# Kernel optimization log

Hardware: AMD Instinct MI355X
Metric: run time of the kernel (lower is better)

The kernel has to match this reference:

```python
import jax, jax.numpy as jnp
import numpy as np

N_X, DIS, IN, OUT = 40000, 10000, 128, 64
N = N_X + DIS
E = 800000
BN_EPS = 1e-5


def setup_inputs() -> dict:
    key = jax.random.key(0)
    ks = jax.random.split(key, 20)

    def glorot(k, shape):
        fan_in, fan_out = shape[-2], shape[-1]
        a = np.sqrt(6.0 / (fan_in + fan_out)).astype(np.float32)
        return jax.random.uniform(k, shape, jnp.float32, -a, a)

    return {
        "x": jax.random.normal(ks[0], (N_X, IN), jnp.float32),
        "emb": jax.random.uniform(ks[1], (DIS, IN), jnp.float32),
        "conv1_w": glorot(ks[2], (3, IN, 2 * OUT)),
        "conv1_root": glorot(ks[3], (IN, 2 * OUT)),
        "conv1_bias": jnp.zeros((2 * OUT,), jnp.float32),
        "conv2_w": glorot(ks[4], (3, 2 * OUT, 4 * OUT)),
        "conv2_root": glorot(ks[5], (2 * OUT, 4 * OUT)),
        "conv2_bias": jnp.zeros((4 * OUT,), jnp.float32),
        "convinf_w": glorot(ks[6], (3, 4 * OUT, 4 * OUT)),
        "convinf_root": glorot(ks[7], (4 * OUT, 4 * OUT)),
        "convinf_bias": jnp.zeros((4 * OUT,), jnp.float32),
        "conv3_w": glorot(ks[8], (3, 4 * OUT, OUT)),
        "conv3_root": glorot(ks[9], (4 * OUT, OUT)),
        "conv3_bias": jnp.zeros((OUT,), jnp.float32),
        "norm1_g": jnp.ones((2 * OUT,), jnp.float32),
        "norm1_b": jnp.zeros((2 * OUT,), jnp.float32),
        "norm2_g": jnp.ones((4 * OUT,), jnp.float32),
        "norm2_b": jnp.zeros((4 * OUT,), jnp.float32),
        "edge_index": jax.random.randint(ks[10], (2, E), 0, N),
        "edge_types": jax.random.randint(ks[11], (E,), 0, 3),
    }


def reference(x, emb, conv1_w, conv1_root, conv1_bias, conv2_w, conv2_root,
              conv2_bias, convinf_w, convinf_root, convinf_bias, conv3_w,
              conv3_root, conv3_bias, norm1_g, norm1_b, norm2_g, norm2_b,
              edge_index, edge_types):
    dst, src = edge_index[0], edge_index[1]  # adj_t row = target, col = source
    n = x.shape[0] + emb.shape[0]

    # gcn_norm without self-loops: deg over rows, w_e = d^-1/2[dst] * d^-1/2[src]
    deg = jax.ops.segment_sum(jnp.ones(dst.shape[0], jnp.float32), dst, num_segments=n)
    dis = jnp.where(deg > 0, jax.lax.rsqrt(jnp.maximum(deg, 1.0)), 0.0)
    ew = dis[dst] * dis[src]  # [E]

    def wrgcn(h, W, root, bias):
        out = h @ root + bias
        h_src = h[src]  # [E, d] gather (dominant memory traffic)
        for r in range(3):
            w_r = jnp.where(edge_types == r, ew, 0.0)
            agg = jax.ops.segment_sum(w_r[:, None] * h_src, dst, num_segments=n)
            out = out + agg @ W[r]
        return out

    def bn(h, g, b):
        m = h.mean(axis=0)
        v = jnp.var(h, axis=0)  # biased, matches torch BN training normalization
        return (h - m) * jax.lax.rsqrt(v + BN_EPS) * g + b

    h0 = jnp.concatenate([x, emb], axis=0)  # [N, IN]
    x1 = bn(wrgcn(h0, conv1_w, conv1_root, conv1_bias), norm1_g, norm1_b)
    x2 = bn(wrgcn(jax.nn.relu(x1), conv2_w, conv2_root, conv2_bias), norm2_g, norm2_b)
    for _ in range(5):
        x2 = bn(wrgcn(jax.nn.relu(x2), convinf_w, convinf_root, convinf_bias), norm2_g, norm2_b)
    return wrgcn(jax.nn.relu(x2), conv3_w, conv3_root, conv3_bias)
```

## Files before the change

kernel.cpp:

```cpp
#include <hip/hip_runtime.h>

#define N_X  40000
#define NN   50000
#define NE   800000
#define MPAD 50048

using short8  = __attribute__((ext_vector_type(8))) short;
using floatx4 = __attribute__((ext_vector_type(4))) float;
using uintx2  = __attribute__((ext_vector_type(2))) unsigned int;
using uintx4  = __attribute__((ext_vector_type(4))) unsigned int;

typedef const __attribute__((address_space(1))) void gv_t;
typedef __attribute__((address_space(3))) void lv_t;

__device__ __forceinline__ unsigned short f2bf(float f) {
  unsigned u = __float_as_uint(f);
  u += 0x7FFF + ((u >> 16) & 1);
  return (unsigned short)(u >> 16);
}
__device__ __forceinline__ float bf2f(unsigned v) {
  return __uint_as_float(v << 16);
}
__device__ __forceinline__ float h2f(unsigned v) {
  unsigned short s = (unsigned short)v;
  _Float16 f;
  __builtin_memcpy(&f, &s, 2);
  return (float)f;
}
__device__ __forceinline__ unsigned short f2h(float f) {
  _Float16 h = (_Float16)f;
  unsigned short s;
  __builtin_memcpy(&s, &h, 2);
  return s;
}

__global__ void k_deg(const int* __restrict__ dst, int* __restrict__ deg) {
  int e = blockIdx.x * blockDim.x + threadIdx.x;
  if (e < NE) atomicAdd(&deg[dst[e]], 1);
}

__global__ void k_dis(const int* __restrict__ deg, float* __restrict__ dis) {
  int i = blockIdx.x * blockDim.x + threadIdx.x;
  if (i < NN) dis[i] = deg[i] > 0 ? rsqrtf((float)deg[i]) : 0.f;
}

#define SCAN_B 1024
#define SCAN_NB 49
__global__ void k_scan1(const int* __restrict__ deg, int* __restrict__ rowp,
                        int* __restrict__ bsum) {
  __shared__ int buf[SCAN_B];
  int b = blockIdx.x;
  int i = b * SCAN_B + threadIdx.x;
  int v = (i < NN) ? deg[i] : 0;
  buf[threadIdx.x] = v;
  __syncthreads();
  for (int off = 1; off < SCAN_B; off <<= 1) {
    int t = (threadIdx.x >= off) ? buf[threadIdx.x - off] : 0;
    __syncthreads();
    buf[threadIdx.x] += t;
    __syncthreads();
  }
  if (i < NN) rowp[i] = buf[threadIdx.x] - v;
  if (threadIdx.x == SCAN_B - 1) bsum[b] = buf[SCAN_B - 1];
}

__global__ void k_scan2(int* __restrict__ bsum) {
  if (threadIdx.x == 0) {
    int acc = 0;
    for (int i = 0; i < SCAN_NB; ++i) { int t = bsum[i]; bsum[i] = acc; acc += t; }
  }
}

__global__ void k_scan3(int* __restrict__ rowp, const int* __restrict__ bsum) {
  int i = blockIdx.x * blockDim.x + threadIdx.x;
  if (i < NN) rowp[i] += bsum[i >> 10];
  if (i == 0) rowp[NN] = NE;
}

__global__ void k_build(const int* __restrict__ dst, const int* __restrict__ src,
                        const int* __restrict__ typ, const float* __restrict__ dis,
                        const int* __restrict__ rowp, int* __restrict__ cur,
                        uintx2* __restrict__ ed) {
  int e = blockIdx.x * blockDim.x + threadIdx.x;
  if (e >= NE) return;
  int d = dst[e], s = src[e];
  int p = rowp[d] + atomicAdd(&cur[d], 1);
  uintx2 v;
  v.x = (unsigned)s | ((unsigned)typ[e] << 28);
  v.y = __float_as_uint(dis[d] * dis[s]);
  ed[p] = v;
}

__global__ void k_prep0(const float* __restrict__ x, const float* __restrict__ emb,
                        unsigned short* __restrict__ Gh, unsigned short* __restrict__ Gl) {
  int idx = blockIdx.x * blockDim.x + threadIdx.x;
  if (idx >= NN * 32) return;
  int r = idx >> 5;
  const float* srcp = (r < N_X) ? (x + (size_t)idx * 4)
                                : (emb + ((size_t)idx - (size_t)N_X * 32) * 4);
  float4 hv = *(const float4*)srcp;
  float vv[4] = {hv.x, hv.y, hv.z, hv.w};
  unsigned hw[2], lw[2];
#pragma unroll
  for (int q = 0; q < 2; ++q) {
    unsigned short h0 = f2bf(vv[2 * q]), h1 = f2bf(vv[2 * q + 1]);
    unsigned short l0 = f2bf(vv[2 * q] - bf2f(h0)), l1 = f2bf(vv[2 * q + 1] - bf2f(h1));
    hw[q] = (unsigned)h0 | ((unsigned)h1 << 16);
    lw[q] = (unsigned)l0 | ((unsigned)l1 << 16);
  }
  size_t o = (size_t)idx * 4;
  *(uintx2*)(Gh + o) = uintx2{hw[0], hw[1]};
  *(uintx2*)(Gl + o) = uintx2{lw[0], lw[1]};
}

__global__ void k_prep(const unsigned short* __restrict__ Hb,
                       const float* __restrict__ bns, const float* __restrict__ g,
                       const float* __restrict__ b, unsigned short* __restrict__ Gh,
                       unsigned short* __restrict__ Gl, int din) {
  int idx = blockIdx.x * blockDim.x + threadIdx.x;
  if (idx >= NN * (din >> 3)) return;
  int c8 = (idx & ((din >> 3) - 1)) * 8;
  uintx4 hv = *(const uintx4*)(Hb + (size_t)idx * 8);
  unsigned hwv[4] = {hv.x, hv.y, hv.z, hv.w};
  unsigned hw[4], lw[4];
#pragma unroll
  for (int q = 0; q < 4; ++q) {
    unsigned short oo[2];
#pragma unroll
    for (int p = 0; p < 2; ++p) {
      int c = c8 + 2 * q + p;
      float mean = bns[c] * (1.f / NN);
      float var = bns[din + c] * (1.f / NN) - mean * mean;
      float rs = rsqrtf(var + 1e-5f);
      float sc = rs * g[c];
      float sh = b[c] - mean * sc;
      float v = bf2f((hwv[q] >> (16 * p)) & 0xFFFFu);
      v = fmaxf(v * sc + sh, 0.f);
      oo[p] = f2bf(v);
      float lo = v - bf2f(oo[p]);
      if (p == 0) lw[q] = (unsigned)f2bf(lo);
      else        lw[q] |= ((unsigned)f2bf(lo) << 16);
    }
    hw[q] = (unsigned)oo[0] | ((unsigned)oo[1] << 16);
  }
  size_t o = (size_t)idx * 8;
  *(uintx4*)(Gh + o) = uintx4{hw[0], hw[1], hw[2], hw[3]};
  *(uintx4*)(Gl + o) = uintx4{lw[0], lw[1], lw[2], lw[3]};
}

__global__ void k_wcat2(const float* __restrict__ root, const float* __restrict__ W,
                        unsigned short* __restrict__ BhT, unsigned short* __restrict__ BlT,
                        int din, int dout) {
  int idx = blockIdx.x * blockDim.x + threadIdx.x;
  if (idx >= 4 * dout * din) return;
  int n = idx / din, k = idx % din;
  float v;
  if (n < dout) v = root[(size_t)k * dout + n];
  else {
    int r = n / dout - 1, c = n % dout;
    v = W[((size_t)r * din + k) * dout + c];
  }
  unsigned short h = f2bf(v);
  BhT[idx] = h;
  BlT[idx] = f2bf(v - bf2f(h));
}

__global__ __launch_bounds__(256, 2) void k_gemm2(
    const unsigned short* __restrict__ Ah, const unsigned short* __restrict__ Al,
    const unsigned short* __restrict__ Bh, const unsigned short* __restrict__ Bl,
    float* __restrict__ Rroot, unsigned short* __restrict__ P,
    int M, int K, int dout, int ny) {
  constexpr int TC = 40;
  constexpr int CPW = 10;
  constexpr int NT = 2;
  __shared__ __align__(16) char lds[2][TC * 1024];

  const int tid = threadIdx.x;
  const int lane = tid & 63;
  const int w = tid >> 6;
  const int wm = w >> 1, wn = w & 1;
  const int r16 = lane & 15, kg = lane >> 4;

  const int nwg = gridDim.x;
  const int q = nwg >> 3, r = nwg & 7;
  const int xcd = blockIdx.x & 7, pos = blockIdx.x >> 3;
  const int t = (xcd < r ? xcd * (q + 1) : r * (q + 1) + (xcd - r) * q) + pos;
  const int bm = (t / ny) * 256;
  const int bn = (t % ny) * 64;

  const int rowseg = lane >> 2;
  const int seg = (lane & 3) ^ ((lane >> 3) & 3);
  const unsigned short* gb[CPW];
#pragma unroll
  for (int i = 0; i < CPW; ++i) {
    int c = w * CPW + i;
    const unsigned short* base;
    int row0;
    if (c < 16)      { base = Ah; row0 = bm + c * 16; }
    else if (c < 32) { base = Al; row0 = bm + (c - 16) * 16; }
    else if (c < 36) { base = Bh; row0 = bn + (c - 32) * 16; }
    else             { base = Bl; row0 = bn + (c - 36) * 16; }
    gb[i] = base + (size_t)(row0 + rowseg) * K + seg * 8;
  }

  floatx4 acc[8][NT];
#pragma unroll
  for (int i = 0; i < 8; ++i)
#pragma unroll
    for (int jj = 0; jj < NT; ++jj) acc[i][jj] = (floatx4)0.f;

  const int nk = K >> 5;

  auto stage = [&](int b, int tk) {
#pragma unroll
    for (int i = 0; i < CPW; ++i)
      __builtin_amdgcn_global_load_lds((gv_t*)(gb[i] + tk * 32),
                                       (lv_t*)&lds[b][(w * CPW + i) * 1024],
                                       16, 0, 0);
  };

  stage(0, 0);
  stage(1, 1);

  const int fo = r16 * 64 + ((kg ^ ((r16 >> 1) & 3)) * 16);

  int buf = 0;
  for (int tk = 0; tk < nk; ++tk) {
    if (tk < nk - 1) asm volatile("s_waitcnt vmcnt(10)" ::: "memory");
    else             asm volatile("s_waitcnt vmcnt(0)" ::: "memory");
    __builtin_amdgcn_s_barrier();

    const char* Lb = lds[buf];
    short8 bh[NT], bl[NT];
#pragma unroll
    for (int nt = 0; nt < NT; ++nt) {
      bh[nt] = *(const short8*)(Lb + (32 + wn * NT + nt) * 1024 + fo);
      bl[nt] = *(const short8*)(Lb + (36 + wn * NT + nt) * 1024 + fo);
    }

    __builtin_amdgcn_s_setprio(1);
#pragma unroll
    for (int mt = 0; mt < 8; ++mt) {
      short8 ah = *(const short8*)(Lb + (wm * 8 + mt) * 1024 + fo);
      short8 al = *(const short8*)(Lb + (16 + wm * 8 + mt) * 1024 + fo);
#pragma unroll
      for (int nt = 0; nt < NT; ++nt) {
        acc[mt][nt] = __builtin_amdgcn_mfma_f32_16x16x32_bf16(ah, bh[nt], acc[mt][nt], 0, 0, 0);
        acc[mt][nt] = __builtin_amdgcn_mfma_f32_16x16x32_bf16(ah, bl[nt], acc[mt][nt], 0, 0, 0);
        acc[mt][nt] = __builtin_amdgcn_mfma_f32_16x16x32_bf16(al, bh[nt], acc[mt][nt], 0, 0, 0);
      }
    }
    __builtin_amdgcn_s_setprio(0);

    __builtin_amdgcn_s_barrier();
    if (tk + 2 < nk) stage(buf, tk + 2);
    buf ^= 1;
  }

  const int sec = bn / dout;
  const int cb = bn - sec * dout;
#pragma unroll
  for (int mt = 0; mt < 8; ++mt) {
    const int gr0 = bm + wm * 128 + mt * 16 + kg * 4;
#pragma unroll
    for (int nt = 0; nt < NT; ++nt) {
      const int colL = cb + wn * 32 + nt * 16 + r16;
#pragma unroll
      for (int rr = 0; rr < 4; ++rr) {
        const int gr = gr0 + rr;
        if (gr >= M) continue;
        const float o = acc[mt][nt][rr];
        if (sec == 0) Rroot[(size_t)gr * dout + colL] = o;
        else          P[((size_t)gr * 3 + (sec - 1)) * dout + colL] = f2h(o);
      }
    }
  }
}

template <int L, bool F32OUT>
__global__ void k_agg2(const unsigned short* __restrict__ P,
                       const float* __restrict__ Rroot,
                       const float* __restrict__ bias,
                       const int* __restrict__ rowp, const uintx2* __restrict__ ed,
                       void* __restrict__ OutV) {
  constexpr int G = 64 / L;
  constexpr int dout = L * 8;
  const int wid = (blockIdx.x * 256 + threadIdx.x) >> 6;
  if (wid >= NN) return;
  const int lane = threadIdx.x & 63;
  const int grp = lane / L;
  const int c0 = (lane & (L - 1)) * 8;
  const int beg = rowp[wid], end = rowp[wid + 1];
  float a[8] = {};
  for (int i = beg + grp; i < end; i += G) {
    const uintx2 e = ed[i];
    const float wv = __uint_as_float(e.y);
    const unsigned tt = e.x >> 28;
    const size_t off = ((size_t)(e.x & 0x0FFFFFFFu) * 3 + tt) * dout + c0;
    const uintx4 g = *(const uintx4*)(P + off);
    a[0] += wv * h2f(g.x & 0xFFFFu);
    a[1] += wv * h2f(g.x >> 16);
    a[2] += wv * h2f(g.y & 0xFFFFu);
    a[3] += wv * h2f(g.y >> 16);
    a[4] += wv * h2f(g.z & 0xFFFFu);
    a[5] += wv * h2f(g.z >> 16);
    a[6] += wv * h2f(g.w & 0xFFFFu);
    a[7] += wv * h2f(g.w >> 16);
  }
#pragma unroll
  for (int off = L; off < 64; off <<= 1) {
#pragma unroll
    for (int qq = 0; qq < 8; ++qq) a[qq] += __shfl_xor(a[qq], off);
  }
  if (grp == 0) {
    const size_t ob = (size_t)wid * dout + c0;
    const float4 bv0 = *(const float4*)(bias + c0);
    const float4 bv1 = *(const float4*)(bias + c0 + 4);
    const float4 rv0 = *(const float4*)(Rroot + ob);
    const float4 rv1 = *(const float4*)(Rroot + ob + 4);
    float o[8];
    o[0] = rv0.x + bv0.x + a[0];
    o[1] = rv0.y + bv0.y + a[1];
    o[2] = rv0.z + bv0.z + a[2];
    o[3] = rv0.w + bv0.w + a[3];
    o[4] = rv1.x + bv1.x + a[4];
    o[5] = rv1.y + bv1.y + a[5];
    o[6] = rv1.z + bv1.z + a[6];
    o[7] = rv1.w + bv1.w + a[7];
    if constexpr (F32OUT) {
      float* Out = (float*)OutV;
      *(float4*)(Out + ob) = make_float4(o[0], o[1], o[2], o[3]);
      *(float4*)(Out + ob + 4) = make_float4(o[4], o[5], o[6], o[7]);
    } else {
      unsigned short* Out = (unsigned short*)OutV;
      uintx4 pk;
      pk.x = (unsigned)f2bf(o[0]) | ((unsigned)f2bf(o[1]) << 16);
      pk.y = (unsigned)f2bf(o[2]) | ((unsigned)f2bf(o[3]) << 16);
      pk.z = (unsigned)f2bf(o[4]) | ((unsigned)f2bf(o[5]) << 16);
      pk.w = (unsigned)f2bf(o[6]) | ((unsigned)f2bf(o[7]) << 16);
      *(uintx4*)(Out + ob) = pk;
    }
  }
}

__global__ void k_bnstats(const unsigned short* __restrict__ Hb,
                          float* __restrict__ sums, int d) {
  __shared__ float ls[512];
  const int cg = d >> 3;
  const int rpb = 256 / cg;
  const int cgi = threadIdx.x & (cg - 1);
  const int rl = threadIdx.x / cg;
  const int c0 = cgi * 8;
  for (int i = threadIdx.x; i < 512; i += 256) ls[i] = 0.f;
  __syncthreads();

  float s[8] = {}, s2[8] = {};
  for (int row = blockIdx.x * rpb + rl; row < NN; row += gridDim.x * rpb) {
    uintx4 hv = *(const uintx4*)(Hb + (size_t)row * d + c0);
    unsigned wv[4] = {hv.x, hv.y, hv.z, hv.w};
#pragma unroll
    for (int q = 0; q < 4; ++q) {
      float v0 = bf2f(wv[q] & 0xFFFFu);
      float v1 = bf2f(wv[q] >> 16);
      s[2 * q] += v0;  s2[2 * q] += v0 * v0;
      s[2 * q + 1] += v1;  s2[2 * q + 1] += v1 * v1;
    }
  }
#pragma unroll
  for (int q = 0; q < 8; ++q) {
    atomicAdd(&ls[c0 + q], s[q]);
    atomicAdd(&ls[256 + c0 + q], s2[q]);
  }
  __syncthreads();
  if (threadIdx.x < d) {
    atomicAdd(&sums[threadIdx.x], ls[threadIdx.x]);
    atomicAdd(&sums[d + threadIdx.x], ls[256 + threadIdx.x]);
  }
}

extern "C" void kernel_launch(void* const* d_in, const int* in_sizes, int n_in,
                              void* d_out, int out_size, void* d_ws, size_t ws_size,
                              hipStream_t stream) {
  const float* x   = (const float*)d_in[0];
  const float* emb = (const float*)d_in[1];
  const float* conv_w[4] = {(const float*)d_in[2], (const float*)d_in[5],
                            (const float*)d_in[8], (const float*)d_in[11]};
  const float* conv_r[4] = {(const float*)d_in[3], (const float*)d_in[6],
                            (const float*)d_in[9], (const float*)d_in[12]};
  const float* conv_b[4] = {(const float*)d_in[4], (const float*)d_in[7],
                            (const float*)d_in[10], (const float*)d_in[13]};
  const float* n1g = (const float*)d_in[14];
  const float* n1b = (const float*)d_in[15];
  const float* n2g = (const float*)d_in[16];
  const float* n2b = (const float*)d_in[17];
  const int* eidx = (const int*)d_in[18];
  const int* etyp = (const int*)d_in[19];
  const int* dst  = eidx;
  const int* srcp = eidx + NE;
  float* out = (float*)d_out;

  char* w = (char*)d_ws;
  auto alloc = [&](size_t bytes) {
    char* p = w;
    w += (bytes + 255) & ~(size_t)255;
    return p;
  };
  unsigned short* Gh   = (unsigned short*)alloc((size_t)MPAD * 256 * 2);
  unsigned short* Gl   = (unsigned short*)alloc((size_t)MPAD * 256 * 2);
  unsigned short* P    = (unsigned short*)alloc((size_t)MPAD * 768 * 2);
  float*    Rroot = (float*)alloc((size_t)MPAD * 256 * 4);
  unsigned short* Hb = (unsigned short*)alloc((size_t)NN * 256 * 2);
  unsigned short* WTh[4];
  unsigned short* WTl[4];
  for (int i = 0; i < 4; ++i) {
    WTh[i] = (unsigned short*)alloc((size_t)1024 * 256 * 2);
    WTl[i] = (unsigned short*)alloc((size_t)1024 * 256 * 2);
  }
  float*    bns  = (float*)alloc(512 * 4);
  float*    dis  = (float*)alloc((size_t)NN * 4);
  int*      deg  = (int*)alloc((size_t)NN * 4);
  int*      rowp = (int*)alloc((size_t)(NN + 1) * 4);
  int*      cur  = (int*)alloc((size_t)NN * 4);
  int*      bsum = (int*)alloc(64 * 4);
  uintx2*   ed   = (uintx2*)alloc((size_t)NE * 8);

  hipMemsetAsync(deg, 0, (size_t)NN * 4, stream);
  hipMemsetAsync(cur, 0, (size_t)NN * 4, stream);
  k_deg<<<(NE + 255) / 256, 256, 0, stream>>>(dst, deg);
  k_dis<<<(NN + 255) / 256, 256, 0, stream>>>(deg, dis);
  k_scan1<<<SCAN_NB, SCAN_B, 0, stream>>>(deg, rowp, bsum);
  k_scan2<<<1, 64, 0, stream>>>(bsum);
  k_scan3<<<(NN + 255) / 256, 256, 0, stream>>>(rowp, bsum);
  k_build<<<(NE + 255) / 256, 256, 0, stream>>>(dst, srcp, etyp, dis, rowp, cur, ed);

  const int din_a[8]  = {128, 128, 256, 256, 256, 256, 256, 256};
  const int dout_a[8] = {128, 256, 256, 256, 256, 256, 256, 64};
  const int wi_a[8]   = {0, 1, 2, 2, 2, 2, 2, 3};
  const int gm = (MPAD + 255) / 256;

  const int wdin[4]  = {128, 128, 256, 256};
  const int wdout[4] = {128, 256, 256, 64};
  for (int i = 0; i < 4; ++i)
    k_wcat2<<<(4 * wdout[i] * wdin[i] + 255) / 256, 256, 0, stream>>>(
        conv_r[i], conv_w[i], WTh[i], WTl[i], wdin[i], wdout[i]);

  for (int l = 0; l < 8; ++l) {
    const int din = din_a[l], dout = dout_a[l];
    const int wi = wi_a[l];

    if (l == 0)
      k_prep0<<<(NN * 32 + 255) / 256, 256, 0, stream>>>(x, emb, Gh, Gl);
    else
      k_prep<<<(NN * (din >> 3) + 255) / 256, 256, 0, stream>>>(
          Hb, bns, (l == 1) ? n1g : n2g, (l == 1) ? n1b : n2b, Gh, Gl, din);

    const int ny = 4 * dout / 64;
    k_gemm2<<<gm * ny, 256, 0, stream>>>(Gh, Gl, WTh[wi], WTl[wi], Rroot, P, NN, din, dout, ny);

    if (l == 7) {
      k_agg2<8, true><<<(NN + 3) / 4, 256, 0, stream>>>(P, Rroot, conv_b[wi], rowp, ed, out);
    } else {
      if (dout == 256)
        k_agg2<32, false><<<(NN + 3) / 4, 256, 0, stream>>>(P, Rroot, conv_b[wi], rowp, ed, Hb);
      else
        k_agg2<16, false><<<(NN + 3) / 4, 256, 0, stream>>>(P, Rroot, conv_b[wi], rowp, ed, Hb);
      hipMemsetAsync(bns, 0, (size_t)2 * dout * 4, stream);
      k_bnstats<<<256, 256, 0, stream>>>(Hb, bns, dout);
    }
  }
}
```

Before: 1.488 ms.

## Widen GEMM tile to 256x128 with 512 threads and triple-buffered LDS

Replaces the 256x64 split-bf16 GEMM with a 256x128 tile run by 8 waves, a three-stage LDS ring buffer and a fully unrolled K loop templated on the K-tile count. Each K step is split into four phases that interleave fragment loads, prefetch of the next stage and MFMA bursts, with barriers between phases. The intent is to halve A-tile reloads per output column and overlap global loads with compute better. The cost is more LDS per block (one block per CU), extra barriers, and sector/column indexing computed per n-tile.

```diff
diff --git a/kernel.cpp b/kernel.cpp
--- a/kernel.cpp
+++ b/kernel.cpp
@@ -165,20 +165,21 @@
   BlT[idx] = f2bf(v - bf2f(h));
 }
 
-__global__ __launch_bounds__(256, 2) void k_gemm2(
+template <int NK>
+__global__ __launch_bounds__(512, 1) void k_gemm4(
     const unsigned short* __restrict__ Ah, const unsigned short* __restrict__ Al,
     const unsigned short* __restrict__ Bh, const unsigned short* __restrict__ Bl,
     float* __restrict__ Rroot, unsigned short* __restrict__ P,
-    int M, int K, int dout, int ny) {
-  constexpr int TC = 40;
-  constexpr int CPW = 10;
-  constexpr int NT = 2;
-  __shared__ __align__(16) char lds[2][TC * 1024];
+    int M, int dout, int ny) {
+  constexpr int K = NK * 32;
+  constexpr int TC = 48;
+  constexpr int CPW = 6;
+  __shared__ __align__(16) char lds[3][TC * 1024];
 
   const int tid = threadIdx.x;
   const int lane = tid & 63;
   const int w = tid >> 6;
-  const int wm = w >> 1, wn = w & 1;
+  const int wm = w >> 2, wn = w & 3;
   const int r16 = lane & 15, kg = lane >> 4;
 
   const int nwg = gridDim.x;
@@ -186,7 +187,7 @@
   const int xcd = blockIdx.x & 7, pos = blockIdx.x >> 3;
   const int t = (xcd < r ? xcd * (q + 1) : r * (q + 1) + (xcd - r) * q) + pos;
   const int bm = (t / ny) * 256;
-  const int bn = (t % ny) * 64;
+  const int bn = (t % ny) * 128;
 
   const int rowseg = lane >> 2;
   const int seg = (lane & 3) ^ ((lane >> 3) & 3);
@@ -198,18 +199,16 @@
     int row0;
     if (c < 16)      { base = Ah; row0 = bm + c * 16; }
     else if (c < 32) { base = Al; row0 = bm + (c - 16) * 16; }
-    else if (c < 36) { base = Bh; row0 = bn + (c - 32) * 16; }
-    else             { base = Bl; row0 = bn + (c - 36) * 16; }
+    else if (c < 40) { base = Bh; row0 = bn + (c - 32) * 16; }
+    else             { base = Bl; row0 = bn + (c - 40) * 16; }
     gb[i] = base + (size_t)(row0 + rowseg) * K + seg * 8;
   }
 
-  floatx4 acc[8][NT];
+  floatx4 acc[8][2];
 #pragma unroll
   for (int i = 0; i < 8; ++i)
 #pragma unroll
-    for (int jj = 0; jj < NT; ++jj) acc[i][jj] = (floatx4)0.f;
-
-  const int nk = K >> 5;
+    for (int jj = 0; jj < 2; ++jj) acc[i][jj] = (floatx4)0.f;
 
   auto stage = [&](int b, int tk) {
 #pragma unroll
@@ -224,47 +223,49 @@
 
   const int fo = r16 * 64 + ((kg ^ ((r16 >> 1) & 3)) * 16);
 
-  int buf = 0;
-  for (int tk = 0; tk < nk; ++tk) {
-    if (tk < nk - 1) asm volatile("s_waitcnt vmcnt(10)" ::: "memory");
+#pragma unroll
+  for (int tk = 0; tk < NK; ++tk) {
+    if (tk < NK - 1) asm volatile("s_waitcnt vmcnt(6)" ::: "memory");
     else             asm volatile("s_waitcnt vmcnt(0)" ::: "memory");
-    __builtin_amdgcn_s_barrier();
-
-    const char* Lb = lds[buf];
-    short8 bh[NT], bl[NT];
-#pragma unroll
-    for (int nt = 0; nt < NT; ++nt) {
-      bh[nt] = *(const short8*)(Lb + (32 + wn * NT + nt) * 1024 + fo);
-      bl[nt] = *(const short8*)(Lb + (36 + wn * NT + nt) * 1024 + fo);
-    }
-
-    __builtin_amdgcn_s_setprio(1);
-#pragma unroll
-    for (int mt = 0; mt < 8; ++mt) {
-      short8 ah = *(const short8*)(Lb + (wm * 8 + mt) * 1024 + fo);
-      short8 al = *(const short8*)(Lb + (16 + wm * 8 + mt) * 1024 + fo);
-#pragma unroll
-      for (int nt = 0; nt < NT; ++nt) {
-        acc[mt][nt] = __builtin_amdgcn_mfma_f32_16x16x32_bf16(ah, bh[nt], acc[mt][nt], 0, 0, 0);
-        acc[mt][nt] = __builtin_amdgcn_mfma_f32_16x16x32_bf16(ah, bl[nt], acc[mt][nt], 0, 0, 0);
-        acc[mt][nt] = __builtin_amdgcn_mfma_f32_16x16x32_bf16(al, bh[nt], acc[mt][nt], 0, 0, 0);
+    __syncthreads();
+
+    const char* Lb = lds[tk % 3];
+    const int sb = (tk + 2) % 3;
+
+#pragma unroll
+    for (int ph = 0; ph < 4; ++ph) {
+      const int m0 = (ph & 1) * 4;
+      const int nt = ph >> 1;
+      short8 afh[4], afl[4];
+#pragma unroll
+      for (int i = 0; i < 4; ++i) {
+        afh[i] = *(const short8*)(Lb + (wm * 8 + m0 + i) * 1024 + fo);
+        afl[i] = *(const short8*)(Lb + (16 + wm * 8 + m0 + i) * 1024 + fo);
       }
-    }
-    __builtin_amdgcn_s_setprio(0);
-
-    __builtin_amdgcn_s_barrier();
-    if (tk + 2 < nk) stage(buf, tk + 2);
-    buf ^= 1;
-  }
-
-  const int sec = bn / dout;
-  const int cb = bn - sec * dout;
+      short8 bfh = *(const short8*)(Lb + (32 + wn * 2 + nt) * 1024 + fo);
+      short8 bfl = *(const short8*)(Lb + (40 + wn * 2 + nt) * 1024 + fo);
+      if (ph == 0 && tk + 2 < NK) stage(sb, tk + 2);
+      __syncthreads();
+      __builtin_amdgcn_s_setprio(1);
+#pragma unroll
+      for (int i = 0; i < 4; ++i) {
+        acc[m0 + i][nt] = __builtin_amdgcn_mfma_f32_16x16x32_bf16(afh[i], bfh, acc[m0 + i][nt], 0, 0, 0);
+        acc[m0 + i][nt] = __builtin_amdgcn_mfma_f32_16x16x32_bf16(afh[i], bfl, acc[m0 + i][nt], 0, 0, 0);
+        acc[m0 + i][nt] = __builtin_amdgcn_mfma_f32_16x16x32_bf16(afl[i], bfh, acc[m0 + i][nt], 0, 0, 0);
+      }
+      __builtin_amdgcn_s_setprio(0);
+      __syncthreads();
+    }
+  }
+
 #pragma unroll
   for (int mt = 0; mt < 8; ++mt) {
     const int gr0 = bm + wm * 128 + mt * 16 + kg * 4;
 #pragma unroll
-    for (int nt = 0; nt < NT; ++nt) {
-      const int colL = cb + wn * 32 + nt * 16 + r16;
+    for (int nt = 0; nt < 2; ++nt) {
+      const int n0 = bn + wn * 32 + nt * 16;
+      const int sec = n0 / dout;
+      const int colL = n0 - sec * dout + r16;
 #pragma unroll
       for (int rr = 0; rr < 4; ++rr) {
         const int gr = gr0 + rr;
@@ -454,8 +455,11 @@
       k_prep<<<(NN * (din >> 3) + 255) / 256, 256, 0, stream>>>(
           Hb, bns, (l == 1) ? n1g : n2g, (l == 1) ? n1b : n2b, Gh, Gl, din);
 
-    const int ny = 4 * dout / 64;
-    k_gemm2<<<gm * ny, 256, 0, stream>>>(Gh, Gl, WTh[wi], WTl[wi], Rroot, P, NN, din, dout, ny);
+    const int ny = 4 * dout / 128;
+    if (din == 128)
+      k_gemm4<4><<<gm * ny, 512, 0, stream>>>(Gh, Gl, WTh[wi], WTl[wi], Rroot, P, NN, dout, ny);
+    else
+      k_gemm4<8><<<gm * ny, 512, 0, stream>>>(Gh, Gl, WTh[wi], WTl[wi], Rroot, P, NN, dout, ny);
 
     if (l == 7) {
       k_agg2<8, true><<<(NN + 3) / 4, 256, 0, stream>>>(P, Rroot, conv_b[wi], rowp, ed, out);
```

Result: slower. 1.740 ms (+17.0%).
